# Optimization experiments

Hardware: AMD Instinct MI355X
Metric: run time of the kernel (lower is better)

## Reference

```python
import jax, jax.numpy as jnp
import numpy as np

H = 2048          # hidden_size
NH = 32           # num_attention_heads
NKV = 8           # num_key_value_heads
HD = H // NH      # head_dim = 64
GROUPS = NH // NKV
B, S = 1, 4096


def setup_inputs() -> dict:
    key = jax.random.key(0)
    k1, k2, k3, k4, k5 = jax.random.split(key, 5)
    hidden_states = jax.random.normal(k1, (B, S, H), dtype=jnp.float32)
    # additive causal mask [B, 1, S, S]
    causal = jnp.tril(jnp.ones((S, S), dtype=bool))
    attention_mask = jnp.where(causal, 0.0, jnp.finfo(jnp.float32).min)[None, None].astype(jnp.float32)
    scale = 0.02
    Wq = jax.random.normal(k2, (H, H), dtype=jnp.float32) * scale
    Wk = jax.random.normal(k3, (NKV * HD, H), dtype=jnp.float32) * scale
    Wv = jax.random.normal(k4, (NKV * HD, H), dtype=jnp.float32) * scale
    Wo = jax.random.normal(k5, (H, H), dtype=jnp.float32) * scale
    return {"hidden_states": hidden_states, "attention_mask": attention_mask,
            "Wq": Wq, "Wk": Wk, "Wv": Wv, "Wo": Wo}


def reference(hidden_states, attention_mask, Wq, Wk, Wv, Wo):
    bsz, q_len, _ = hidden_states.shape
    # projections (nn.Linear: x @ W.T)
    q = (hidden_states @ Wq.T).reshape(bsz, q_len, NH, HD).transpose(0, 2, 1, 3)   # [B,NH,S,HD]
    k = (hidden_states @ Wk.T).reshape(bsz, q_len, NKV, HD).transpose(0, 2, 1, 3)  # [B,NKV,S,HD]
    v = (hidden_states @ Wv.T).reshape(bsz, q_len, NKV, HD).transpose(0, 2, 1, 3)
    # repeat_kv: expand each KV head GROUPS times
    k = jnp.repeat(k, GROUPS, axis=1)  # [B,NH,S,HD]
    v = jnp.repeat(v, GROUPS, axis=1)
    attn_weights = jnp.einsum('bhqd,bhkd->bhqk', q, k) / jnp.sqrt(jnp.float32(HD))
    attn_weights = attn_weights + attention_mask
    attn_weights = jax.nn.softmax(attn_weights.astype(jnp.float32), axis=-1).astype(q.dtype)
    attn_output = jnp.einsum('bhqk,bhkd->bhqd', attn_weights, v)
    attn_output = attn_output.transpose(0, 2, 1, 3).reshape(bsz, q_len, H)
    return attn_output @ Wo.T
```

## Files before the change

kernel.cpp:

```cpp
#include <hip/hip_runtime.h>
#include <stdint.h>

#define S_LEN  4096
#define HDIM   2048
#define NHEADS 32
#define NKVH   8
#define HDSZ   64
#define KVDIM  (NKVH * HDSZ)
#define QKN    (HDIM + KVDIM)

typedef __bf16 v8bf16 __attribute__((ext_vector_type(8)));
typedef short  v4s    __attribute__((ext_vector_type(4)));
typedef float  v4f32  __attribute__((ext_vector_type(4)));

__device__ __forceinline__ unsigned short f2bf(float f) {
    uint32_t u = __builtin_bit_cast(uint32_t, f);
    uint32_t r = (u + 0x7fffu + ((u >> 16) & 1u)) >> 16;
    return (unsigned short)r;
}

__device__ __forceinline__ uint32_t pack_bf16(float a, float b) {
#if __has_builtin(__builtin_amdgcn_cvt_pk_bf16_f32)
    auto r = __builtin_amdgcn_cvt_pk_bf16_f32(a, b);
    return __builtin_bit_cast(uint32_t, r);
#else
    uint32_t ua = __builtin_bit_cast(uint32_t, a) + 0x8000u;
    uint32_t ub = __builtin_bit_cast(uint32_t, b) + 0x8000u;
    return (ua >> 16) | (ub & 0xffff0000u);
#endif
}

__device__ __forceinline__ float fast_exp2(float x) {
#if __has_builtin(__builtin_amdgcn_exp2f)
    return __builtin_amdgcn_exp2f(x);
#else
    float r; asm("v_exp_f32 %0, %1" : "=v"(r) : "v"(x)); return r;
#endif
}

__device__ __forceinline__ void async_load16(const void* g, void* l) {
    __builtin_amdgcn_global_load_lds((const __attribute__((address_space(1))) void*)g,
                                     (__attribute__((address_space(3))) void*)l,
                                     16, 0, 0);
}

#define SEG0 2097152
#define SEG1 3145728
#define SEG2 3407872
#define SEG3 3670016
#define SEGT 4718592
__global__ void cvt_all(const float* __restrict__ x,  const float* __restrict__ wq,
                        const float* __restrict__ wk, const float* __restrict__ wv,
                        const float* __restrict__ wo,
                        ushort4* __restrict__ xb, ushort4* __restrict__ wqkb,
                        ushort4* __restrict__ wvb, ushort4* __restrict__ wob,
                        float qscale)
{
    int i = blockIdx.x * blockDim.x + threadIdx.x;
    if (i >= SEGT) return;
    const float4* src; ushort4* dst; float s = 1.0f; int loc;
    if (i < SEG0)      { src = (const float4*)x;  dst = xb;   loc = i; }
    else if (i < SEG1) { src = (const float4*)wq; dst = wqkb; loc = i - SEG0; s = qscale; }
    else if (i < SEG2) { src = (const float4*)wk; dst = wqkb + 1048576; loc = i - SEG1; }
    else if (i < SEG3) { src = (const float4*)wv; dst = wvb;  loc = i - SEG2; }
    else               { src = (const float4*)wo; dst = wob;  loc = i - SEG3; }
    float4 f = src[loc];
    uint2 o;
    o.x = pack_bf16(f.x * s, f.y * s);
    o.y = pack_bf16(f.z * s, f.w * s);
    dst[loc] = __builtin_bit_cast(ushort4, o);
}

__device__ __forceinline__ void gemm_tile_body(
    const unsigned short* __restrict__ A, const unsigned short* __restrict__ B,
    unsigned short* __restrict__ C, int N, int K, int m0, int n0,
    unsigned short* As, unsigned short* Bs)
{
    const int tid  = threadIdx.x;
    const int wave = tid >> 6;
    const int lane = tid & 63;
    const int lrow = lane & 15;
    const int quad = lane >> 4;
    const int wm = (wave >> 1) * 64;
    const int wn = (wave & 1) * 64;

    const int srow = wave * 32 + (lane >> 3);
    const int sg   = (lane & 7) ^ ((lane >> 3) & 7);
    const size_t aOff = (size_t)(m0 + srow) * K + sg * 8;
    const size_t bOff = (size_t)(n0 + srow) * K + sg * 8;

    v4f32 acc[4][4];
#pragma unroll
    for (int mi = 0; mi < 4; ++mi)
#pragma unroll
        for (int ni = 0; ni < 4; ++ni)
#pragma unroll
            for (int r = 0; r < 4; ++r) acc[mi][ni][r] = 0.0f;

    for (int k0 = 0; k0 < K; k0 += 64) {
#pragma unroll
        for (int i = 0; i < 4; ++i) {
            async_load16(A + aOff + (size_t)(i * 8) * K + k0,
                         &As[(wave * 32 + i * 8) * 64]);
            async_load16(B + bOff + (size_t)(i * 8) * K + k0,
                         &Bs[(wave * 32 + i * 8) * 64]);
        }
        __syncthreads();
#pragma unroll
        for (int ks = 0; ks < 2; ++ks) {
            const int kg  = ks * 4 + quad;
            const int swz = (kg ^ (lrow & 7)) * 8;
            v8bf16 af[4], bfm[4];
#pragma unroll
            for (int mi = 0; mi < 4; ++mi)
                af[mi] = *(const v8bf16*)&As[(wm + mi * 16 + lrow) * 64 + swz];
#pragma unroll
            for (int ni = 0; ni < 4; ++ni)
                bfm[ni] = *(const v8bf16*)&Bs[(wn + ni * 16 + lrow) * 64 + swz];
#pragma unroll
            for (int mi = 0; mi < 4; ++mi)
#pragma unroll
                for (int ni = 0; ni < 4; ++ni)
                    acc[mi][ni] = __builtin_amdgcn_mfma_f32_16x16x32_bf16(
                        af[mi], bfm[ni], acc[mi][ni], 0, 0, 0);
        }
        __syncthreads();
    }

#pragma unroll
    for (int mi = 0; mi < 4; ++mi)
#pragma unroll
        for (int ni = 0; ni < 4; ++ni)
#pragma unroll
            for (int r = 0; r < 4; ++r) {
                const int row = m0 + wm + mi * 16 + quad * 4 + r;
                const int col = n0 + wn + ni * 16 + lrow;
                C[(size_t)row * N + col] = f2bf(acc[mi][ni][r]);
            }
}

__global__ __launch_bounds__(256)
void gemm_qkv(const unsigned short* __restrict__ xb,
              const unsigned short* __restrict__ Wqkb,
              const unsigned short* __restrict__ Wvb,
              unsigned short* __restrict__ QKb,
              unsigned short* __restrict__ Vtb)
{
    __shared__ unsigned short As[128 * 64];
    __shared__ unsigned short Bs[128 * 64];
    const int bid = blockIdx.x;
    if (bid < 128) {
        gemm_tile_body(Wvb, xb, Vtb, S_LEN, HDIM,
                       (bid & 3) * 128, (bid >> 2) * 128, As, Bs);
    } else {
        const int b = bid - 128;
        gemm_tile_body(xb, Wqkb, QKb, QKN, HDIM,
                       (b & 31) * 128, (b >> 5) * 128, As, Bs);
    }
}

__global__ __launch_bounds__(256)
void gemm_bt_f32(const unsigned short* __restrict__ A,
                 const unsigned short* __restrict__ B,
                 float* __restrict__ Cout, int M, int N, int K)
{
    __shared__ unsigned short As[128 * 64];
    __shared__ unsigned short Bs[128 * 64];

    const int tid  = threadIdx.x;
    const int wave = tid >> 6;
    const int lane = tid & 63;
    const int lrow = lane & 15;
    const int quad = lane >> 4;

    const int m0 = blockIdx.x * 128;
    const int n0 = blockIdx.y * 128;
    const int wm = (wave >> 1) * 64;
    const int wn = (wave & 1) * 64;

    const int srow = wave * 32 + (lane >> 3);
    const int sg   = (lane & 7) ^ ((lane >> 3) & 7);
    const size_t aOff = (size_t)(m0 + srow) * K + sg * 8;
    const size_t bOff = (size_t)(n0 + srow) * K + sg * 8;

    v4f32 acc[4][4];
#pragma unroll
    for (int mi = 0; mi < 4; ++mi)
#pragma unroll
        for (int ni = 0; ni < 4; ++ni)
#pragma unroll
            for (int r = 0; r < 4; ++r) acc[mi][ni][r] = 0.0f;

    for (int k0 = 0; k0 < K; k0 += 64) {
#pragma unroll
        for (int i = 0; i < 4; ++i) {
            async_load16(A + aOff + (size_t)(i * 8) * K + k0,
                         &As[(wave * 32 + i * 8) * 64]);
            async_load16(B + bOff + (size_t)(i * 8) * K + k0,
                         &Bs[(wave * 32 + i * 8) * 64]);
        }
        __syncthreads();
#pragma unroll
        for (int ks = 0; ks < 2; ++ks) {
            const int kg  = ks * 4 + quad;
            const int swz = (kg ^ (lrow & 7)) * 8;
            v8bf16 af[4], bfm[4];
#pragma unroll
            for (int mi = 0; mi < 4; ++mi)
                af[mi] = *(const v8bf16*)&As[(wm + mi * 16 + lrow) * 64 + swz];
#pragma unroll
            for (int ni = 0; ni < 4; ++ni)
                bfm[ni] = *(const v8bf16*)&Bs[(wn + ni * 16 + lrow) * 64 + swz];
#pragma unroll
            for (int mi = 0; mi < 4; ++mi)
#pragma unroll
                for (int ni = 0; ni < 4; ++ni)
                    acc[mi][ni] = __builtin_amdgcn_mfma_f32_16x16x32_bf16(
                        af[mi], bfm[ni], acc[mi][ni], 0, 0, 0);
        }
        __syncthreads();
    }

#pragma unroll
    for (int mi = 0; mi < 4; ++mi)
#pragma unroll
        for (int ni = 0; ni < 4; ++ni)
#pragma unroll
            for (int r = 0; r < 4; ++r) {
                const int row = m0 + wm + mi * 16 + quad * 4 + r;
                const int col = n0 + wn + ni * 16 + lrow;
                Cout[(size_t)row * N + col] = acc[mi][ni][r];
            }
}

__global__ __launch_bounds__(256, 4)
void flash_attn(const unsigned short* __restrict__ QK,
                const unsigned short* __restrict__ Vt,
                unsigned short* __restrict__ O)
{
    __shared__ unsigned short smem[16384];
    unsigned short* Qs = smem;
    unsigned short* Ks = smem + 128 * 64;
    unsigned short* Vs = smem + 128 * 64 + 64 * 64;

    const int tid  = threadIdx.x;
    const int wave = tid >> 6;
    const int lane = tid & 63;
    const int lrow = lane & 15;
    const int quad = lane >> 4;

    const int h   = blockIdx.x;
    const int kvh = h >> 2;
    const int q0  = (gridDim.y - 1 - blockIdx.y) * 128;

    const int srow8 = lane >> 3;
    const int sgrp  = (lane & 7) ^ srow8;
    const v8bf16 v_one8 = __builtin_bit_cast(v8bf16,
        (uint4){0x3F803F80u, 0x3F803F80u, 0x3F803F80u, 0x3F803F80u});

    {
        const size_t gq = (size_t)(q0 + wave * 32 + srow8) * QKN + h * HDSZ + sgrp * 8;
#pragma unroll
        for (int i = 0; i < 4; ++i)
            async_load16(QK + gq + (size_t)(i * 8) * QKN, &Qs[(wave * 32 + i * 8) * 64]);
    }

    int kperm[2];
#pragma unroll
    for (int i = 0; i < 2; ++i) {
        const int slot = wave * 16 + i * 8 + srow8;
        const int nj = slot >> 4, sm = slot & 15;
        kperm[i] = 32 * (nj >> 1) + 8 * (sm >> 2) + 4 * (nj & 1) + (sm & 3);
    }

    v4f32 o_acc[2][4], l_acc[2];
#pragma unroll
    for (int mi = 0; mi < 2; ++mi) {
#pragma unroll
        for (int r = 0; r < 4; ++r) l_acc[mi][r] = 0.0f;
#pragma unroll
        for (int dj = 0; dj < 4; ++dj)
#pragma unroll
            for (int r = 0; r < 4; ++r) o_acc[mi][dj][r] = 0.0f;
    }

    const int rbase = q0 + wave * 32;
    const int njt   = (q0 >> 6) + 2;

    for (int j = 0; j < njt; ++j) {
        const int k0 = j * 64;
        __syncthreads();
        {
#pragma unroll
            for (int i = 0; i < 2; ++i) {
                const size_t gk = (size_t)(k0 + kperm[i]) * QKN
                                  + HDIM + kvh * HDSZ + sgrp * 8;
                async_load16(QK + gk, &Ks[(wave * 16 + i * 8) * 64]);
            }
            const size_t gv = (size_t)(kvh * HDSZ + wave * 16 + srow8) * S_LEN
                              + k0 + sgrp * 8;
            async_load16(Vt + gv,             &Vs[(wave * 16) * 64]);
            async_load16(Vt + gv + 8 * S_LEN, &Vs[(wave * 16 + 8) * 64]);
        }
        __syncthreads();

        if (k0 > rbase + 31) continue;

        v4f32 st[2][4];
#pragma unroll
        for (int mi = 0; mi < 2; ++mi)
#pragma unroll
            for (int nj = 0; nj < 4; ++nj)
#pragma unroll
                for (int r = 0; r < 4; ++r) st[mi][nj][r] = 0.0f;
#pragma unroll
        for (int kk = 0; kk < 2; ++kk) {
            const int swz = ((kk * 4 + quad) ^ (lrow & 7)) * 8;
            v8bf16 qa[2];
            qa[0] = *(const v8bf16*)&Qs[(wave * 32 + lrow) * 64 + swz];
            qa[1] = *(const v8bf16*)&Qs[(wave * 32 + 16 + lrow) * 64 + swz];
#pragma unroll
            for (int nj = 0; nj < 4; ++nj) {
                const v8bf16 kb = *(const v8bf16*)&Ks[(nj * 16 + lrow) * 64 + swz];
                st[0][nj] = __builtin_amdgcn_mfma_f32_16x16x32_bf16(kb, qa[0], st[0][nj], 0, 0, 0);
                st[1][nj] = __builtin_amdgcn_mfma_f32_16x16x32_bf16(kb, qa[1], st[1][nj], 0, 0, 0);
            }
        }

        if (k0 + 63 > rbase) {
#pragma unroll
            for (int mi = 0; mi < 2; ++mi) {
                const int qi = rbase + mi * 16 + lrow;
#pragma unroll
                for (int nj = 0; nj < 4; ++nj) {
                    const int kib = k0 + 32 * (nj >> 1) + 8 * quad + 4 * (nj & 1);
#pragma unroll
                    for (int r = 0; r < 4; ++r)
                        if (kib + r > qi) st[mi][nj][r] = -1e30f;
                }
            }
        }

        v8bf16 pk8[2][2];
#pragma unroll
        for (int mi = 0; mi < 2; ++mi) {
            uint2 pu[4];
#pragma unroll
            for (int nj = 0; nj < 4; ++nj) {
                const float p0 = fast_exp2(st[mi][nj][0]);
                const float p1 = fast_exp2(st[mi][nj][1]);
                const float p2 = fast_exp2(st[mi][nj][2]);
                const float p3 = fast_exp2(st[mi][nj][3]);
                pu[nj].x = pack_bf16(p0, p1);
                pu[nj].y = pack_bf16(p2, p3);
            }
            pk8[mi][0] = __builtin_bit_cast(v8bf16, (uint4){pu[0].x, pu[0].y, pu[1].x, pu[1].y});
            pk8[mi][1] = __builtin_bit_cast(v8bf16, (uint4){pu[2].x, pu[2].y, pu[3].x, pu[3].y});
        }

#pragma unroll
        for (int t = 0; t < 2; ++t) {
            const int swzv = ((t * 4 + quad) ^ (lrow & 7)) * 8;
            v8bf16 va[4];
#pragma unroll
            for (int dj = 0; dj < 4; ++dj)
                va[dj] = *(const v8bf16*)&Vs[(dj * 16 + lrow) * 64 + swzv];
#pragma unroll
            for (int dj = 0; dj < 4; ++dj) {
                o_acc[0][dj] = __builtin_amdgcn_mfma_f32_16x16x32_bf16(va[dj], pk8[0][t], o_acc[0][dj], 0, 0, 0);
                o_acc[1][dj] = __builtin_amdgcn_mfma_f32_16x16x32_bf16(va[dj], pk8[1][t], o_acc[1][dj], 0, 0, 0);
            }
            l_acc[0] = __builtin_amdgcn_mfma_f32_16x16x32_bf16(v_one8, pk8[0][t], l_acc[0], 0, 0, 0);
            l_acc[1] = __builtin_amdgcn_mfma_f32_16x16x32_bf16(v_one8, pk8[1][t], l_acc[1], 0, 0, 0);
        }
    }

    __syncthreads();
    unsigned short* Os = smem;
#pragma unroll
    for (int mi = 0; mi < 2; ++mi) {
        const float inv = 1.0f / l_acc[mi][0];
#pragma unroll
        for (int dj = 0; dj < 4; ++dj)
#pragma unroll
            for (int r = 0; r < 4; ++r)
                Os[(wave * 32 + mi * 16 + lrow) * 72 + dj * 16 + quad * 4 + r] =
                    f2bf(o_acc[mi][dj][r] * inv);
    }
    __syncthreads();
#pragma unroll
    for (int i = 0; i < 4; ++i) {
        const int idx = i * 256 + tid;
        const int row = idx >> 3, c8 = idx & 7;
        const uint4 vv = *(const uint4*)&Os[row * 72 + c8 * 8];
        *(uint4*)&O[(size_t)(q0 + row) * HDIM + h * HDSZ + c8 * 8] = vv;
    }
}

extern "C" void kernel_launch(void* const* d_in, const int* in_sizes, int n_in,
                              void* d_out, int out_size, void* d_ws, size_t ws_size,
                              hipStream_t stream)
{
    const float* x  = (const float*)d_in[0];
    const float* Wq = (const float*)d_in[2];
    const float* Wk = (const float*)d_in[3];
    const float* Wv = (const float*)d_in[4];
    const float* Wo = (const float*)d_in[5];
    float* out = (float*)d_out;

    unsigned short* xb   = (unsigned short*)d_ws;
    unsigned short* Wqkb = xb   + (size_t)S_LEN * HDIM;
    unsigned short* Wvb  = Wqkb + (size_t)QKN * HDIM;
    unsigned short* Wob  = Wvb  + (size_t)KVDIM * HDIM;
    unsigned short* QKb  = Wob  + (size_t)HDIM * HDIM;
    unsigned short* Vtb  = QKb  + (size_t)S_LEN * QKN;
    unsigned short* AOb  = xb;

    cvt_all<<<(SEGT + 255) / 256, 256, 0, stream>>>(
        x, Wq, Wk, Wv, Wo,
        (ushort4*)xb, (ushort4*)Wqkb, (ushort4*)Wvb, (ushort4*)Wob,
        0.18033688011f);

    gemm_qkv<<<768, 256, 0, stream>>>(xb, Wqkb, Wvb, QKb, Vtb);

    flash_attn<<<dim3(NHEADS, S_LEN / 128), 256, 0, stream>>>(QKb, Vtb, AOb);

    gemm_bt_f32<<<dim3(S_LEN / 128, HDIM / 128), 256, 0, stream>>>(
        AOb, Wob, out, S_LEN, HDIM, HDIM);
}
```

Measured before the change: 346.2 us.

## Replace projection GEMMs with 256x256 double-buffered pipelined MFMA kernel

```diff
diff --git a/kernel.cpp b/kernel.cpp
--- a/kernel.cpp
+++ b/kernel.cpp
@@ -71,166 +71,222 @@
     dst[loc] = __builtin_bit_cast(ushort4, o);
 }
 
-__device__ __forceinline__ void gemm_tile_body(
-    const unsigned short* __restrict__ A, const unsigned short* __restrict__ B,
-    unsigned short* __restrict__ C, int N, int K, int m0, int n0,
-    unsigned short* As, unsigned short* Bs)
+
+#define STAGE_A(buf, kh, t)                                                       \
+    do {                                                                          \
+        async_load16(A + aBase + (size_t)(t) * 64 + (kh) * 32,                    \
+                     &smem[(buf) * 16384 + (kh) * 8192 + ldsSt]);                 \
+        async_load16(A + aBase + (size_t)128 * Kd + (size_t)(t) * 64 + (kh) * 32, \
+                     &smem[(buf) * 16384 + (kh) * 8192 + ldsSt + 4096]);          \
+    } while (0)
+#define STAGE_B(buf, kh, t)                                                       \
+    do {                                                                          \
+        async_load16(Bp + bBase + (size_t)(t) * 64 + (kh) * 32,                   \
+                     &smem[32768 + (buf) * 16384 + (kh) * 8192 + ldsSt]);         \
+        async_load16(Bp + bBase + (size_t)128 * Kd + (size_t)(t) * 64 + (kh) * 32,\
+                     &smem[32768 + (buf) * 16384 + (kh) * 8192 + ldsSt + 4096]);  \
+    } while (0)
+
+#define LOAD_AF(khoff)                                                            \
+    do {                                                                          \
+        _Pragma("unroll")                                                         \
+        for (int mi = 0; mi < 8; ++mi)                                            \
+            af[mi] = *(const v8bf16*)&smem[curA + (khoff) + aRd + mi * 512];      \
+    } while (0)
+
+#define MFMA_PAIR(khoff, NI)                                                      \
+    do {                                                                          \
+        v8bf16 _b0 = *(const v8bf16*)&smem[curB + (khoff) + bRd + (NI) * 512];    \
+        v8bf16 _b1 = *(const v8bf16*)&smem[curB + (khoff) + bRd + (NI) * 512 + 512];\
+        __builtin_amdgcn_s_setprio(1);                                            \
+        _Pragma("unroll")                                                         \
+        for (int mi = 0; mi < 8; ++mi) {                                          \
+            acc[mi][(NI)]     = __builtin_amdgcn_mfma_f32_16x16x32_bf16(af[mi], _b0, acc[mi][(NI)], 0, 0, 0);     \
+            acc[mi][(NI) + 1] = __builtin_amdgcn_mfma_f32_16x16x32_bf16(af[mi], _b1, acc[mi][(NI) + 1], 0, 0, 0); \
+        }                                                                         \
+        __builtin_amdgcn_s_setprio(0);                                            \
+    } while (0)
+
+#define FENCE_BAR()                                                               \
+    do {                                                                          \
+        __builtin_amdgcn_sched_barrier(0);                                        \
+        __builtin_amdgcn_s_barrier();                                             \
+        __builtin_amdgcn_sched_barrier(0);                                        \
+    } while (0)
+
+#define WAITV(N) asm volatile("s_waitcnt vmcnt(" #N ")" ::: "memory")
+
+template<bool F32OUT>
+__device__ __forceinline__ void gemm256_body(
+    const unsigned short* __restrict__ A,
+    const unsigned short* __restrict__ Bp,
+    void* __restrict__ Cout, int Nn, int Kd, int m0, int n0,
+    unsigned short* __restrict__ smem)
 {
     const int tid  = threadIdx.x;
     const int wave = tid >> 6;
     const int lane = tid & 63;
     const int lrow = lane & 15;
     const int quad = lane >> 4;
-    const int wm = (wave >> 1) * 64;
-    const int wn = (wave & 1) * 64;
-
-    const int srow = wave * 32 + (lane >> 3);
-    const int sg   = (lane & 7) ^ ((lane >> 3) & 7);
-    const size_t aOff = (size_t)(m0 + srow) * K + sg * 8;
-    const size_t bOff = (size_t)(n0 + srow) * K + sg * 8;
-
-    v4f32 acc[4][4];
-#pragma unroll
-    for (int mi = 0; mi < 4; ++mi)
+    const int wm = (wave >> 2) * 128;
+    const int wn = (wave & 3) * 64;
+
+    const int lr   = lane >> 2;
+    const int sg4  = (lane & 3) ^ ((lane >> 3) & 3);
+    const size_t aBase = (size_t)(m0 + wave * 16 + lr) * Kd + sg4 * 8;
+    const size_t bBase = (size_t)(n0 + wave * 16 + lr) * Kd + sg4 * 8;
+    const int ldsSt = wave * 512;
+
+    const int rg4 = (quad ^ ((lrow >> 1) & 3)) * 8;
+    const int aRd = (wm + lrow) * 32 + rg4;
+    const int bRd = (wn + lrow) * 32 + rg4;
+
+    const int NT = Kd >> 6;
+
+    v4f32 acc[8][4];
+#pragma unroll
+    for (int mi = 0; mi < 8; ++mi)
 #pragma unroll
         for (int ni = 0; ni < 4; ++ni)
 #pragma unroll
             for (int r = 0; r < 4; ++r) acc[mi][ni][r] = 0.0f;
 
-    for (int k0 = 0; k0 < K; k0 += 64) {
-#pragma unroll
-        for (int i = 0; i < 4; ++i) {
-            async_load16(A + aOff + (size_t)(i * 8) * K + k0,
-                         &As[(wave * 32 + i * 8) * 64]);
-            async_load16(B + bOff + (size_t)(i * 8) * K + k0,
-                         &Bs[(wave * 32 + i * 8) * 64]);
-        }
-        __syncthreads();
-#pragma unroll
-        for (int ks = 0; ks < 2; ++ks) {
-            const int kg  = ks * 4 + quad;
-            const int swz = (kg ^ (lrow & 7)) * 8;
-            v8bf16 af[4], bfm[4];
-#pragma unroll
-            for (int mi = 0; mi < 4; ++mi)
-                af[mi] = *(const v8bf16*)&As[(wm + mi * 16 + lrow) * 64 + swz];
+    STAGE_A(0, 0, 0); STAGE_B(0, 0, 0);
+    STAGE_A(0, 1, 0); STAGE_B(0, 1, 0);
+    STAGE_A(1, 0, 1); STAGE_B(1, 0, 1);
+    WAITV(8);
+    __builtin_amdgcn_s_barrier();
+    __builtin_amdgcn_sched_barrier(0);
+
+    v8bf16 af[8];
+    for (int t = 0; t < NT - 2; ++t) {
+        const int cur  = t & 1;
+        const int nxt  = cur ^ 1;
+        const int curA = cur * 16384;
+        const int curB = 32768 + cur * 16384;
+
+        STAGE_A(nxt, 1, t + 1);
+        LOAD_AF(0);
+        MFMA_PAIR(0, 0);
+        FENCE_BAR();
+
+        STAGE_B(nxt, 1, t + 1);
+        MFMA_PAIR(0, 2);
+        WAITV(8);
+        FENCE_BAR();
+
+        STAGE_A(cur, 0, t + 2);
+        LOAD_AF(8192);
+        MFMA_PAIR(8192, 0);
+        FENCE_BAR();
+
+        STAGE_B(cur, 0, t + 2);
+        MFMA_PAIR(8192, 2);
+        WAITV(8);
+        FENCE_BAR();
+    }
+
+    {
+        const int t = NT - 2;
+        const int cur  = t & 1;
+        const int nxt  = cur ^ 1;
+        const int curA = cur * 16384;
+        const int curB = 32768 + cur * 16384;
+
+        STAGE_A(nxt, 1, t + 1);
+        LOAD_AF(0);
+        MFMA_PAIR(0, 0);
+        FENCE_BAR();
+
+        STAGE_B(nxt, 1, t + 1);
+        MFMA_PAIR(0, 2);
+        WAITV(8);
+        FENCE_BAR();
+
+        LOAD_AF(8192);
+        MFMA_PAIR(8192, 0);
+        FENCE_BAR();
+
+        MFMA_PAIR(8192, 2);
+        WAITV(4);
+        FENCE_BAR();
+    }
+
+    {
+        const int cur  = (NT - 1) & 1;
+        const int curA = cur * 16384;
+        const int curB = 32768 + cur * 16384;
+
+        LOAD_AF(0);
+        MFMA_PAIR(0, 0);
+        FENCE_BAR();
+
+        MFMA_PAIR(0, 2);
+        WAITV(0);
+        FENCE_BAR();
+
+        LOAD_AF(8192);
+        MFMA_PAIR(8192, 0);
+        FENCE_BAR();
+
+        MFMA_PAIR(8192, 2);
+    }
+
+    if (F32OUT) {
+        float* Cf = (float*)Cout;
+#pragma unroll
+        for (int mi = 0; mi < 8; ++mi)
 #pragma unroll
             for (int ni = 0; ni < 4; ++ni)
-                bfm[ni] = *(const v8bf16*)&Bs[(wn + ni * 16 + lrow) * 64 + swz];
-#pragma unroll
-            for (int mi = 0; mi < 4; ++mi)
-#pragma unroll
-                for (int ni = 0; ni < 4; ++ni)
-                    acc[mi][ni] = __builtin_amdgcn_mfma_f32_16x16x32_bf16(
-                        af[mi], bfm[ni], acc[mi][ni], 0, 0, 0);
-        }
-        __syncthreads();
-    }
-
-#pragma unroll
-    for (int mi = 0; mi < 4; ++mi)
-#pragma unroll
-        for (int ni = 0; ni < 4; ++ni)
-#pragma unroll
-            for (int r = 0; r < 4; ++r) {
-                const int row = m0 + wm + mi * 16 + quad * 4 + r;
-                const int col = n0 + wn + ni * 16 + lrow;
-                C[(size_t)row * N + col] = f2bf(acc[mi][ni][r]);
-            }
-}
-
-__global__ __launch_bounds__(256)
-void gemm_qkv(const unsigned short* __restrict__ xb,
-              const unsigned short* __restrict__ Wqkb,
-              const unsigned short* __restrict__ Wvb,
-              unsigned short* __restrict__ QKb,
-              unsigned short* __restrict__ Vtb)
-{
-    __shared__ unsigned short As[128 * 64];
-    __shared__ unsigned short Bs[128 * 64];
+#pragma unroll
+                for (int r = 0; r < 4; ++r) {
+                    const int row = m0 + wm + mi * 16 + quad * 4 + r;
+                    const int col = n0 + wn + ni * 16 + lrow;
+                    Cf[(size_t)row * Nn + col] = acc[mi][ni][r];
+                }
+    } else {
+        unsigned short* Cb = (unsigned short*)Cout;
+#pragma unroll
+        for (int mi = 0; mi < 8; ++mi)
+#pragma unroll
+            for (int ni = 0; ni < 4; ++ni)
+#pragma unroll
+                for (int r = 0; r < 4; ++r) {
+                    const int row = m0 + wm + mi * 16 + quad * 4 + r;
+                    const int col = n0 + wn + ni * 16 + lrow;
+                    Cb[(size_t)row * Nn + col] = f2bf(acc[mi][ni][r]);
+                }
+    }
+}
+
+__global__ __launch_bounds__(512, 2)
+void gemm_qkv256(const unsigned short* __restrict__ xb,
+                 const unsigned short* __restrict__ Wqkb,
+                 const unsigned short* __restrict__ Wvb,
+                 unsigned short* __restrict__ QKb,
+                 unsigned short* __restrict__ Vtb)
+{
+    __shared__ __align__(16) unsigned short smem[65536];
     const int bid = blockIdx.x;
-    if (bid < 128) {
-        gemm_tile_body(Wvb, xb, Vtb, S_LEN, HDIM,
-                       (bid & 3) * 128, (bid >> 2) * 128, As, Bs);
+    if (bid < 32) {
+        gemm256_body<false>(Wvb, xb, Vtb, S_LEN, HDIM,
+                            (bid >> 4) * 256, (bid & 15) * 256, smem);
     } else {
-        const int b = bid - 128;
-        gemm_tile_body(xb, Wqkb, QKb, QKN, HDIM,
-                       (b & 31) * 128, (b >> 5) * 128, As, Bs);
-    }
-}
-
-__global__ __launch_bounds__(256)
-void gemm_bt_f32(const unsigned short* __restrict__ A,
-                 const unsigned short* __restrict__ B,
-                 float* __restrict__ Cout, int M, int N, int K)
-{
-    __shared__ unsigned short As[128 * 64];
-    __shared__ unsigned short Bs[128 * 64];
-
-    const int tid  = threadIdx.x;
-    const int wave = tid >> 6;
-    const int lane = tid & 63;
-    const int lrow = lane & 15;
-    const int quad = lane >> 4;
-
-    const int m0 = blockIdx.x * 128;
-    const int n0 = blockIdx.y * 128;
-    const int wm = (wave >> 1) * 64;
-    const int wn = (wave & 1) * 64;
-
-    const int srow = wave * 32 + (lane >> 3);
-    const int sg   = (lane & 7) ^ ((lane >> 3) & 7);
-    const size_t aOff = (size_t)(m0 + srow) * K + sg * 8;
-    const size_t bOff = (size_t)(n0 + srow) * K + sg * 8;
-
-    v4f32 acc[4][4];
-#pragma unroll
-    for (int mi = 0; mi < 4; ++mi)
-#pragma unroll
-        for (int ni = 0; ni < 4; ++ni)
-#pragma unroll
-            for (int r = 0; r < 4; ++r) acc[mi][ni][r] = 0.0f;
-
-    for (int k0 = 0; k0 < K; k0 += 64) {
-#pragma unroll
-        for (int i = 0; i < 4; ++i) {
-            async_load16(A + aOff + (size_t)(i * 8) * K + k0,
-                         &As[(wave * 32 + i * 8) * 64]);
-            async_load16(B + bOff + (size_t)(i * 8) * K + k0,
-                         &Bs[(wave * 32 + i * 8) * 64]);
-        }
-        __syncthreads();
-#pragma unroll
-        for (int ks = 0; ks < 2; ++ks) {
-            const int kg  = ks * 4 + quad;
-            const int swz = (kg ^ (lrow & 7)) * 8;
-            v8bf16 af[4], bfm[4];
-#pragma unroll
-            for (int mi = 0; mi < 4; ++mi)
-                af[mi] = *(const v8bf16*)&As[(wm + mi * 16 + lrow) * 64 + swz];
-#pragma unroll
-            for (int ni = 0; ni < 4; ++ni)
-                bfm[ni] = *(const v8bf16*)&Bs[(wn + ni * 16 + lrow) * 64 + swz];
-#pragma unroll
-            for (int mi = 0; mi < 4; ++mi)
-#pragma unroll
-                for (int ni = 0; ni < 4; ++ni)
-                    acc[mi][ni] = __builtin_amdgcn_mfma_f32_16x16x32_bf16(
-                        af[mi], bfm[ni], acc[mi][ni], 0, 0, 0);
-        }
-        __syncthreads();
-    }
-
-#pragma unroll
-    for (int mi = 0; mi < 4; ++mi)
-#pragma unroll
-        for (int ni = 0; ni < 4; ++ni)
-#pragma unroll
-            for (int r = 0; r < 4; ++r) {
-                const int row = m0 + wm + mi * 16 + quad * 4 + r;
-                const int col = n0 + wn + ni * 16 + lrow;
-                Cout[(size_t)row * N + col] = acc[mi][ni][r];
-            }
+        const int b = bid - 32;
+        gemm256_body<false>(xb, Wqkb, QKb, QKN, HDIM,
+                            (b & 15) * 256, (b >> 4) * 256, smem);
+    }
+}
+
+__global__ __launch_bounds__(512, 2)
+void gemm_o256(const unsigned short* __restrict__ A,
+               const unsigned short* __restrict__ B,
+               float* __restrict__ Cout)
+{
+    __shared__ __align__(16) unsigned short smem[65536];
+    const int bid = blockIdx.x;
+    gemm256_body<true>(A, B, Cout, HDIM, HDIM,
+                       (bid & 15) * 256, (bid >> 4) * 256, smem);
 }
 
 __global__ __launch_bounds__(256, 4)
@@ -421,10 +477,9 @@
         (ushort4*)xb, (ushort4*)Wqkb, (ushort4*)Wvb, (ushort4*)Wob,
         0.18033688011f);
 
-    gemm_qkv<<<768, 256, 0, stream>>>(xb, Wqkb, Wvb, QKb, Vtb);
+    gemm_qkv256<<<192, 512, 0, stream>>>(xb, Wqkb, Wvb, QKb, Vtb);
 
     flash_attn<<<dim3(NHEADS, S_LEN / 128), 256, 0, stream>>>(QKb, Vtb, AOb);
 
-    gemm_bt_f32<<<dim3(S_LEN / 128, HDIM / 128), 256, 0, stream>>>(
-        AOb, Wob, out, S_LEN, HDIM, HDIM);
-}
+    gemm_o256<<<128, 512, 0, stream>>>(AOb, Wob, out);
+}
```

Result: no change. 343.5 us (-0.8%).
